# Performance work log

Hardware: AMD Instinct MI355X
Metric: run time of the kernel (lower is better)

## Reference

```python
import jax, jax.numpy as jnp
import numpy as np

D = 2048
N_EXPERTS = 64
K = 2


def setup_inputs() -> dict:
    key = jax.random.key(0)
    kx, kw = jax.random.split(key)
    x = jax.random.normal(kx, (4, 4096, D), dtype=jnp.float32)
    # xavier_uniform for Linear(d, n_experts): bound = sqrt(6/(fan_in+fan_out))
    bound = float(np.sqrt(6.0 / (D + N_EXPERTS)))
    W = jax.random.uniform(kw, (N_EXPERTS, D), dtype=jnp.float32, minval=-bound, maxval=bound)
    b = jnp.zeros((N_EXPERTS,), dtype=jnp.float32)
    return {"x": x, "W": W, "b": b}


def reference(x, W, b):
    # logits: [B, S, E]  (eval mode: no noise)
    logits = jnp.einsum("bsd,ed->bse", x, W) + b
    topk_vals, topk_idx = jax.lax.top_k(logits, K)  # [B, S, K]
    gates = jax.nn.softmax(topk_vals, axis=-1)
    return gates, topk_idx
```

## Files before the change

kernel.cpp:

```cpp
#include <hip/hip_runtime.h>
#include <math.h>

#define DD 2048
#define EE 64
#define TM 64
#define BK 64
#define NCHUNK (DD / BK)
#define THREADS 256
#define LDSTR (TM + 4)

__global__ __launch_bounds__(THREADS) void router_kernel(
    const float* __restrict__ x, const float* __restrict__ W,
    const float* __restrict__ bias_g, float* __restrict__ out, int n_tokens)
{
    __shared__ float xs[BK * LDSTR];
    __shared__ float ws[BK * LDSTR];
    __shared__ float logits[TM * (EE + 1)];

    const int tid = threadIdx.x;
    const int tx  = tid & 15;
    const int ty  = tid >> 4;
    const int tBase = blockIdx.x * TM;

    const float* xg = x + (size_t)tBase * DD;

    float acc[4][4];
#pragma unroll
    for (int i = 0; i < 4; ++i)
#pragma unroll
        for (int j = 0; j < 4; ++j) acc[i][j] = 0.f;

    float bvals[4];
#pragma unroll
    for (int j = 0; j < 4; ++j) bvals[j] = bias_g[tx * 4 + j];

    float4 rx[4], rw[4];

#define LOAD_TILES(k0)                                                        \
    {                                                                         \
        _Pragma("unroll")                                                     \
        for (int p = 0; p < 4; ++p) {                                         \
            rx[p] = *(const float4*)&xg[(size_t)(ty + 16 * p) * DD + (k0) + tx * 4]; \
            rw[p] = *(const float4*)&W [(size_t)(ty + 16 * p) * DD + (k0) + tx * 4]; \
        }                                                                     \
    }

    LOAD_TILES(0);

    for (int c = 0; c < NCHUNK; ++c) {
        __syncthreads();
#pragma unroll
        for (int p = 0; p < 4; ++p) {
            const int col = ty + 16 * p;
            const int kk  = tx * 4;
            xs[(kk + 0) * LDSTR + col] = rx[p].x;
            xs[(kk + 1) * LDSTR + col] = rx[p].y;
            xs[(kk + 2) * LDSTR + col] = rx[p].z;
            xs[(kk + 3) * LDSTR + col] = rx[p].w;
            ws[(kk + 0) * LDSTR + col] = rw[p].x;
            ws[(kk + 1) * LDSTR + col] = rw[p].y;
            ws[(kk + 2) * LDSTR + col] = rw[p].z;
            ws[(kk + 3) * LDSTR + col] = rw[p].w;
        }
        __syncthreads();

        if (c + 1 < NCHUNK) {
            const int k0n = (c + 1) * BK;
            LOAD_TILES(k0n);
        }

#pragma unroll
        for (int k = 0; k < BK; ++k) {
            const float4 xv = *(const float4*)&xs[k * LDSTR + ty * 4];
            const float4 wv = *(const float4*)&ws[k * LDSTR + tx * 4];
            acc[0][0] += xv.x * wv.x; acc[0][1] += xv.x * wv.y;
            acc[0][2] += xv.x * wv.z; acc[0][3] += xv.x * wv.w;
            acc[1][0] += xv.y * wv.x; acc[1][1] += xv.y * wv.y;
            acc[1][2] += xv.y * wv.z; acc[1][3] += xv.y * wv.w;
            acc[2][0] += xv.z * wv.x; acc[2][1] += xv.z * wv.y;
            acc[2][2] += xv.z * wv.z; acc[2][3] += xv.z * wv.w;
            acc[3][0] += xv.w * wv.x; acc[3][1] += xv.w * wv.y;
            acc[3][2] += xv.w * wv.z; acc[3][3] += xv.w * wv.w;
        }
    }

    __syncthreads();
#pragma unroll
    for (int i = 0; i < 4; ++i)
#pragma unroll
        for (int j = 0; j < 4; ++j)
            logits[(ty * 4 + i) * (EE + 1) + (tx * 4 + j)] = acc[i][j] + bvals[j];
    __syncthreads();

    if (tid < TM) {
        const float* lrow = &logits[tid * (EE + 1)];
        float v1 = -INFINITY, v2 = -INFINITY;
        int   i1 = 0, i2 = 0;
        for (int e = 0; e < EE; ++e) {
            const float v = lrow[e];
            if (v > v1) { v2 = v1; i2 = i1; v1 = v; i1 = e; }
            else if (v > v2) { v2 = v; i2 = e; }
        }
        const float ed = expf(v2 - v1);
        const float inv = 1.f / (1.f + ed);
        const int tok = tBase + tid;
        out[tok * 2 + 0] = inv;
        out[tok * 2 + 1] = ed * inv;
        float* oidx = out + (size_t)2 * n_tokens;
        oidx[tok * 2 + 0] = (float)i1;
        oidx[tok * 2 + 1] = (float)i2;
    }
}

extern "C" void kernel_launch(void* const* d_in, const int* in_sizes, int n_in,
                              void* d_out, int out_size, void* d_ws, size_t ws_size,
                              hipStream_t stream) {
    const float* x = (const float*)d_in[0];
    const float* W = (const float*)d_in[1];
    const float* b = (const float*)d_in[2];
    float* out = (float*)d_out;

    const int n_tokens = in_sizes[0] / DD;
    const int n_blocks = n_tokens / TM;

    router_kernel<<<n_blocks, THREADS, 0, stream>>>(x, W, b, out, n_tokens);
}
```

Measured before the change: 246.3 us.

## Double-buffer tiles via direct global-to-LDS loads with XOR swizzle

Replaces the register-staged, transposed LDS tile fill with __builtin_amdgcn_global_load_lds, which writes global data straight into double-buffered LDS tiles stored row-major with an XOR swizzle to avoid bank conflicts. The main loop issues the next chunk's loads before computing on the current buffer and uses explicit s_waitcnt/s_barrier. The compute loop reads float4s along k and maps each thread's outputs strided by 16. The aim is to remove the register round-trip and the LDS transpose stores, and to overlap memory with compute. In exchange it relies on hand-counted vmcnt values and doubles LDS use, which may lower occupancy.

```diff
diff --git a/kernel.cpp b/kernel.cpp
--- a/kernel.cpp
+++ b/kernel.cpp
@@ -7,20 +7,25 @@
 #define BK 64
 #define NCHUNK (DD / BK)
 #define THREADS 256
-#define LDSTR (TM + 4)
+#define LSTR (EE + 1)
 
 __global__ __launch_bounds__(THREADS) void router_kernel(
     const float* __restrict__ x, const float* __restrict__ W,
     const float* __restrict__ bias_g, float* __restrict__ out, int n_tokens)
 {
-    __shared__ float xs[BK * LDSTR];
-    __shared__ float ws[BK * LDSTR];
-    __shared__ float logits[TM * (EE + 1)];
+    __shared__ float xs[2][TM * BK];
+    __shared__ float ws[2][EE * BK];
+    __shared__ float logits[TM * LSTR];
 
-    const int tid = threadIdx.x;
-    const int tx  = tid & 15;
-    const int ty  = tid >> 4;
+    const int tid   = threadIdx.x;
+    const int lane  = tid & 63;
+    const int wv_id = tid >> 6;
+    const int tx    = tid & 15;
+    const int ty    = tid >> 4;
     const int tBase = blockIdx.x * TM;
+
+    const int rg = lane >> 4;
+    const int p  = lane & 15;
 
     const float* xg = x + (size_t)tBase * DD;
 
@@ -30,70 +35,75 @@
 #pragma unroll
         for (int j = 0; j < 4; ++j) acc[i][j] = 0.f;
 
+    const int xswz = ty & 7;
+    const int wswz = tx & 7;
+
+    auto stage = [&](int buf, int c) {
+        const int k0 = c * BK;
+#pragma unroll
+        for (int i = 0; i < 4; ++i) {
+            const int row = 16 * wv_id + 4 * i + rg;
+            const int qc  = p ^ (row & 7);
+            const float* gx = xg + (size_t)row * DD + k0 + 4 * qc;
+            const float* gw = W  + (size_t)row * DD + k0 + 4 * qc;
+            __builtin_amdgcn_global_load_lds(
+                (const __attribute__((address_space(1))) void*)gx,
+                (__attribute__((address_space(3))) void*)&xs[buf][(16 * wv_id + 4 * i) * BK],
+                16, 0, 0);
+            __builtin_amdgcn_global_load_lds(
+                (const __attribute__((address_space(1))) void*)gw,
+                (__attribute__((address_space(3))) void*)&ws[buf][(16 * wv_id + 4 * i) * BK],
+                16, 0, 0);
+        }
+    };
+
+    auto compute = [&](int buf) {
+#pragma unroll
+        for (int k4 = 0; k4 < BK / 4; ++k4) {
+            float4 xv[4], wv[4];
+#pragma unroll
+            for (int i = 0; i < 4; ++i)
+                xv[i] = *(const float4*)&xs[buf][(ty + 16 * i) * BK + 4 * (k4 ^ xswz)];
+#pragma unroll
+            for (int j = 0; j < 4; ++j)
+                wv[j] = *(const float4*)&ws[buf][(tx + 16 * j) * BK + 4 * (k4 ^ wswz)];
+#pragma unroll
+            for (int i = 0; i < 4; ++i)
+#pragma unroll
+                for (int j = 0; j < 4; ++j) {
+                    acc[i][j] += xv[i].x * wv[j].x;
+                    acc[i][j] += xv[i].y * wv[j].y;
+                    acc[i][j] += xv[i].z * wv[j].z;
+                    acc[i][j] += xv[i].w * wv[j].w;
+                }
+        }
+    };
+
+    stage(0, 0);
+    int cur = 0;
+#pragma unroll 1
+    for (int c = 0; c < NCHUNK - 1; ++c) {
+        stage(cur ^ 1, c + 1);
+        asm volatile("s_waitcnt vmcnt(8)\n\ts_barrier" ::: "memory");
+        compute(cur);
+        asm volatile("s_waitcnt lgkmcnt(0)\n\ts_barrier" ::: "memory");
+        cur ^= 1;
+    }
+    asm volatile("s_waitcnt vmcnt(0)\n\ts_barrier" ::: "memory");
+    compute(cur);
+
     float bvals[4];
 #pragma unroll
-    for (int j = 0; j < 4; ++j) bvals[j] = bias_g[tx * 4 + j];
-
-    float4 rx[4], rw[4];
-
-#define LOAD_TILES(k0)                                                        \
-    {                                                                         \
-        _Pragma("unroll")                                                     \
-        for (int p = 0; p < 4; ++p) {                                         \
-            rx[p] = *(const float4*)&xg[(size_t)(ty + 16 * p) * DD + (k0) + tx * 4]; \
-            rw[p] = *(const float4*)&W [(size_t)(ty + 16 * p) * DD + (k0) + tx * 4]; \
-        }                                                                     \
-    }
-
-    LOAD_TILES(0);
-
-    for (int c = 0; c < NCHUNK; ++c) {
-        __syncthreads();
-#pragma unroll
-        for (int p = 0; p < 4; ++p) {
-            const int col = ty + 16 * p;
-            const int kk  = tx * 4;
-            xs[(kk + 0) * LDSTR + col] = rx[p].x;
-            xs[(kk + 1) * LDSTR + col] = rx[p].y;
-            xs[(kk + 2) * LDSTR + col] = rx[p].z;
-            xs[(kk + 3) * LDSTR + col] = rx[p].w;
-            ws[(kk + 0) * LDSTR + col] = rw[p].x;
-            ws[(kk + 1) * LDSTR + col] = rw[p].y;
-            ws[(kk + 2) * LDSTR + col] = rw[p].z;
-            ws[(kk + 3) * LDSTR + col] = rw[p].w;
-        }
-        __syncthreads();
-
-        if (c + 1 < NCHUNK) {
-            const int k0n = (c + 1) * BK;
-            LOAD_TILES(k0n);
-        }
-
-#pragma unroll
-        for (int k = 0; k < BK; ++k) {
-            const float4 xv = *(const float4*)&xs[k * LDSTR + ty * 4];
-            const float4 wv = *(const float4*)&ws[k * LDSTR + tx * 4];
-            acc[0][0] += xv.x * wv.x; acc[0][1] += xv.x * wv.y;
-            acc[0][2] += xv.x * wv.z; acc[0][3] += xv.x * wv.w;
-            acc[1][0] += xv.y * wv.x; acc[1][1] += xv.y * wv.y;
-            acc[1][2] += xv.y * wv.z; acc[1][3] += xv.y * wv.w;
-            acc[2][0] += xv.z * wv.x; acc[2][1] += xv.z * wv.y;
-            acc[2][2] += xv.z * wv.z; acc[2][3] += xv.z * wv.w;
-            acc[3][0] += xv.w * wv.x; acc[3][1] += xv.w * wv.y;
-            acc[3][2] += xv.w * wv.z; acc[3][3] += xv.w * wv.w;
-        }
-    }
-
-    __syncthreads();
+    for (int j = 0; j < 4; ++j) bvals[j] = bias_g[tx + 16 * j];
 #pragma unroll
     for (int i = 0; i < 4; ++i)
 #pragma unroll
         for (int j = 0; j < 4; ++j)
-            logits[(ty * 4 + i) * (EE + 1) + (tx * 4 + j)] = acc[i][j] + bvals[j];
+            logits[(ty + 16 * i) * LSTR + (tx + 16 * j)] = acc[i][j] + bvals[j];
     __syncthreads();
 
     if (tid < TM) {
-        const float* lrow = &logits[tid * (EE + 1)];
+        const float* lrow = &logits[tid * LSTR];
         float v1 = -INFINITY, v2 = -INFINITY;
         int   i1 = 0, i2 = 0;
         for (int e = 0; e < EE; ++e) {
@@ -101,7 +111,7 @@
             if (v > v1) { v2 = v1; i2 = i1; v1 = v; i1 = e; }
             else if (v > v2) { v2 = v; i2 = e; }
         }
-        const float ed = expf(v2 - v1);
+        const float ed  = expf(v2 - v1);
         const float inv = 1.f / (1.f + ed);
         const int tok = tBase + tid;
         out[tok * 2 + 0] = inv;
```

After: 268.9 us. 9.2% more time.
